# Kernel tuning notes

Hardware: AMD Instinct MI355X
Metric: run time of the kernel (lower is better)

Reference implementation:

```python
import jax, jax.numpy as jnp
import numpy as np

N_E, E_DIM, BETA = 8192, 512, 0.25


def setup_inputs() -> dict:
    key = jax.random.key(0)
    k1, k2 = jax.random.split(key)
    z = jax.random.normal(k1, (16, 1024, E_DIM), dtype=jnp.float32)
    # embedding initialized uniform(-1/n_e, 1/n_e)
    emb_w = jax.random.uniform(k2, (N_E, E_DIM), dtype=jnp.float32,
                               minval=-1.0 / N_E, maxval=1.0 / N_E)
    return {"z": z, "emb_w": emb_w}


def reference(z, emb_w):
    B, T, D = z.shape
    zf = z.reshape(-1, D)  # [BT, D]
    # squared-distance matrix: ||z||^2 + ||e||^2 - 2 z e^T  -> [BT, n_e]
    d = (jnp.sum(zf * zf, axis=1, keepdims=True)
         + jnp.sum(emb_w * emb_w, axis=1)
         - 2.0 * jnp.einsum('bd,nd->bn', zf, emb_w))
    idx = jnp.argmin(d, axis=1)  # [BT]
    z_q = emb_w[idx].reshape(z.shape)  # [B, T, D]
    # legacy=False: beta * commit + codebook term
    loss = (BETA * jnp.mean((jax.lax.stop_gradient(z_q) - z) ** 2)
            + jnp.mean((z_q - jax.lax.stop_gradient(z)) ** 2))
    # straight-through: value equals z_q
    z_q_st = z + jax.lax.stop_gradient(z_q - z)
    idx_out = idx.reshape(B, T)
    v = jnp.var(idx_out.astype(jnp.float32))
    return z_q_st, loss, idx_out, v
```

## Files before the change

kernel.cpp:

```cpp
#include <hip/hip_runtime.h>


#define BT   16384
#define DIMS 512
#define NE   8192
#define NS   4
#define BN   256
#define NTPB (NE / NS / BN)
#define NSTEPS 64

#define LOSS_OFF 8388608
#define IDX_OFF  8388609
#define V_OFF    8404993

#define BEST_OFF  0
#define ENORM_OFF 131072
#define SUMS_OFF  163840
#define CNT_OFF   163864

typedef __attribute__((ext_vector_type(8))) short short8;
typedef __attribute__((ext_vector_type(4))) float floatx4;

#define AS1(p) ((const __attribute__((address_space(1))) void*)(p))
#define AS3(p) ((__attribute__((address_space(3))) void*)(p))

__device__ __forceinline__ unsigned f2bf(float f) {
    unsigned u = __builtin_bit_cast(unsigned, f);
    u += 0x7FFFu + ((u >> 16) & 1u);
    return u >> 16;
}

__global__ __launch_bounds__(256) void prep_kernel(
    const float* __restrict__ z, const float* __restrict__ emb,
    ushort* __restrict__ zh, ushort* __restrict__ ehh,
    float* __restrict__ enorm, unsigned long long* __restrict__ best,
    double* __restrict__ sums, unsigned* __restrict__ counter)
{
    const int lane = threadIdx.x & 63, w = threadIdx.x >> 6;
    const int b = blockIdx.x;
    if (b < NE / 4) {
        const int row = b * 4 + w;
        const float4* p = (const float4*)(emb + (size_t)row * DIMS + lane * 8);
        float4 a = p[0], bb = p[1];
        uint4 h;
        h.x = f2bf(a.x) | (f2bf(a.y) << 16);
        h.y = f2bf(a.z) | (f2bf(a.w) << 16);
        h.z = f2bf(bb.x) | (f2bf(bb.y) << 16);
        h.w = f2bf(bb.z) | (f2bf(bb.w) << 16);
        *(uint4*)(ehh + (size_t)row * DIMS + lane * 8) = h;
        float s = a.x*a.x + a.y*a.y + a.z*a.z + a.w*a.w
                + bb.x*bb.x + bb.y*bb.y + bb.z*bb.z + bb.w*bb.w;
        #pragma unroll
        for (int off = 32; off > 0; off >>= 1) s += __shfl_down(s, off, 64);
        if (lane == 0) enorm[row] = s;
    } else {
        const int row = (b - NE / 4) * 4 + w;
        const float4* p = (const float4*)(z + (size_t)row * DIMS + lane * 8);
        float4 a = p[0], bb = p[1];
        uint4 h;
        h.x = f2bf(a.x) | (f2bf(a.y) << 16);
        h.y = f2bf(a.z) | (f2bf(a.w) << 16);
        h.z = f2bf(bb.x) | (f2bf(bb.y) << 16);
        h.w = f2bf(bb.z) | (f2bf(bb.w) << 16);
        *(uint4*)(zh + (size_t)row * DIMS + lane * 8) = h;
    }
    const int gid = b * 256 + threadIdx.x;
    if (gid < BT) best[gid] = 0xFFFFFFFFFFFFFFFFULL;
    if (gid == 0) { sums[0] = 0.0; sums[1] = 0.0; sums[2] = 0.0; *counter = 0u; }
}


#define LOADB(AB_, NJ0)                                                        \
    _Pragma("unroll")                                                          \
    for (int j2 = 0; j2 < 2; j2++) {                                           \
        b[j2][0] = *(const short8*)&lds[16384u + (AB_) + bro + ((NJ0) + j2) * 1024 + pxo0]; \
        b[j2][1] = *(const short8*)&lds[16384u + (AB_) + bro + ((NJ0) + j2) * 1024 + pxo1]; \
    }

#define PHASE_MID(NJ0)                                                         \
    __builtin_amdgcn_sched_barrier(0);                                         \
    __builtin_amdgcn_s_barrier();                                              \
    asm volatile("s_waitcnt lgkmcnt(0)" ::: "memory");                         \
    __builtin_amdgcn_sched_barrier(0);                                         \
    __builtin_amdgcn_s_setprio(1);                                             \
    _Pragma("unroll")                                                          \
    for (int kk = 0; kk < 2; kk++)                                             \
        _Pragma("unroll")                                                      \
        for (int j2 = 0; j2 < 2; j2++)                                         \
            _Pragma("unroll")                                                  \
            for (int mi = 0; mi < 4; mi++)                                     \
                acc[mi][(NJ0) + j2] = __builtin_amdgcn_mfma_f32_16x16x32_bf16( \
                    a[mi][kk], b[j2][kk], acc[mi][(NJ0) + j2], 0, 0, 0);       \
    __builtin_amdgcn_s_setprio(0);

#define STAGE_A(SA_, H_) do {                                                  \
    const int sa_ = (SA_);                                                     \
    if (sa_ < NSTEPS) {                                                        \
        const int k0_ = (sa_ & 7) * 64;                                        \
        const unsigned al_ = (unsigned)(sa_ & 1) * 32768u                      \
                           + (unsigned)((((H_) * 128) + w * 8) * 64);          \
        const ushort* g_ = zA + (size_t)((H_) * 128) * DIMS + soff + k0_;      \
        __builtin_amdgcn_global_load_lds(AS1(g_), AS3(&lds[al_]), 16, 0, 0);   \
        __builtin_amdgcn_global_load_lds(AS1(g_ + (size_t)64 * DIMS),          \
                                         AS3(&lds[al_ + 64 * 64]), 16, 0, 0);  \
    }                                                                          \
} while (0)

#define STAGE_B(SB_, H_) do {                                                  \
    const int sb_ = (SB_);                                                     \
    if (sb_ < NSTEPS) {                                                        \
        const int k0_ = (sb_ & 7) * 64;                                        \
        const unsigned bl_ = 16384u + (unsigned)(sb_ & 1) * 32768u             \
                           + (unsigned)((((H_) * 128) + w * 8) * 64);          \
        const ushort* g_ = eh + (size_t)(nsN + (sb_ >> 3) * 256 + (H_) * 128) * DIMS \
                         + soff + k0_;                                         \
        __builtin_amdgcn_global_load_lds(AS1(g_), AS3(&lds[bl_]), 16, 0, 0);   \
        __builtin_amdgcn_global_load_lds(AS1(g_ + (size_t)64 * DIMS),          \
                                         AS3(&lds[bl_ + 64 * 64]), 16, 0, 0);  \
    }                                                                          \
} while (0)

#define STEP(S_, AB_, TM_) do {                                                \
    const int s_ = (S_);                                                       \
    short8 a[4][2], b[2][2];                                                   \
         \
    _Pragma("unroll")                                                          \
    for (int mi = 0; mi < 4; mi++) {                                           \
        a[mi][0] = *(const short8*)&lds[(AB_) + aro + mi * 1024 + pxo0];       \
        a[mi][1] = *(const short8*)&lds[(AB_) + aro + mi * 1024 + pxo1];       \
    }                                                                          \
    LOADB(AB_, 0)                                                              \
    STAGE_B(s_ + 1, 0);                                                        \
    PHASE_MID(0)                                                               \
    __builtin_amdgcn_s_barrier();                                              \
                                   \
    LOADB(AB_, 2)                                                              \
    STAGE_B(s_ + 1, 1);                                                        \
    PHASE_MID(2)                                                               \
    __builtin_amdgcn_s_barrier();                                              \
      \
    LOADB(AB_, 4)                                                              \
    STAGE_A(s_ + 2, 0);                                                        \
    PHASE_MID(4)                                                               \
    __builtin_amdgcn_s_barrier();                                              \
            \
    LOADB(AB_, 6)                                                              \
    STAGE_A(s_ + 2, 1);                                                        \
    PHASE_MID(6)                                                               \
    if ((TM_) == 0) asm volatile("s_waitcnt vmcnt(4)" ::: "memory");           \
    else if ((TM_) == 1) asm volatile("s_waitcnt vmcnt(0)" ::: "memory");      \
    __builtin_amdgcn_s_barrier();                                              \
} while (0)

__global__ __launch_bounds__(512, 2) void argmin_mfma(
    const ushort* __restrict__ zh, const ushort* __restrict__ eh,
    const float* __restrict__ enorm, unsigned long long* __restrict__ best)
{
    __shared__ __align__(16) ushort lds[69632];
    float* elds = (float*)&lds[65536];

    const int t = threadIdx.x;
    const int w = t >> 6, lane = t & 63;
    const int quad = lane >> 4, l15 = lane & 15;

    const int d = blockIdx.x;
    const int xcd = d & 7, slot = d >> 3;
    const int ns = xcd >> 1;
    const int mt = slot * 2 + (xcd & 1);
    const int m0 = mt * 256;
    const int nsN = ns * (NTPB * BN);

    const int wrow = (w & 3) * 64;
    const int wcol = (w >> 2) * 128;

    {
        float4 v = *(const float4*)(enorm + nsN + t * 4);
        *(float4*)(elds + t * 4) = v;
    }
    __syncthreads();

    const int l8 = lane >> 3, c8 = lane & 7;
    const int chunk = c8 ^ l8;
    const int soff = (w * 8 + l8) * DIMS + chunk * 8;
    const ushort* zA = zh + (size_t)m0 * DIMS;

    const int pxo0 = (quad ^ (l15 & 7)) * 8;
    const int pxo1 = ((4 + quad) ^ (l15 & 7)) * 8;
    const int aro = (wrow + l15) * 64;
    const int bro = (wcol + l15) * 64;

    floatx4 acc[4][8];
    #pragma unroll
    for (int mi = 0; mi < 4; mi++)
        #pragma unroll
        for (int nj = 0; nj < 8; nj++)
            acc[mi][nj] = (floatx4){0.f, 0.f, 0.f, 0.f};

    float bs[16];
    int   bn_[16];
    #pragma unroll
    for (int k = 0; k < 16; k++) { bs[k] = 3.4e38f; bn_[k] = 0; }

    STAGE_A(0, 0); STAGE_A(0, 1);
    STAGE_B(0, 0); STAGE_B(0, 1);
    STAGE_A(1, 0); STAGE_A(1, 1);
    asm volatile("s_waitcnt vmcnt(4)" ::: "memory");
    __builtin_amdgcn_s_barrier();

    for (int sp = 0; sp < NSTEPS; sp += 2) {
        const int tm1 = (sp != NSTEPS - 2) ? 0 : 1;
        const int tm2 = (sp != NSTEPS - 2) ? 0 : 2;
        STEP(sp, 0u, tm1);
        STEP(sp + 1, 32768u, tm2);

        if ((sp & 7) == 6) {
            const int nt = sp >> 3;
            const int ebase = nt * 256 + wcol + l15;
            const int nbase = nsN + nt * 256 + wcol + l15;
            #pragma unroll
            for (int nj = 0; nj < 8; nj++) {
                const float en = elds[ebase + nj * 16];
                const int n = nbase + nj * 16;
                #pragma unroll
                for (int mi = 0; mi < 4; mi++) {
                    #pragma unroll
                    for (int r = 0; r < 4; r++) {
                        const int k = mi * 4 + r;
                        const float sc = fmaf(-2.0f, acc[mi][nj][r], en);
                        if (sc < bs[k]) { bs[k] = sc; bn_[k] = n; }
                    }
                    acc[mi][nj] = (floatx4){0.f, 0.f, 0.f, 0.f};
                }
            }
        }
    }

    #pragma unroll
    for (int mi = 0; mi < 4; mi++)
        #pragma unroll
        for (int r = 0; r < 4; r++) {
            const int k = mi * 4 + r;
            unsigned su = __builtin_bit_cast(unsigned, bs[k]);
            su = (su & 0x80000000u) ? ~su : (su | 0x80000000u);
            unsigned long long key = ((unsigned long long)su << 32) | (unsigned)bn_[k];
            #pragma unroll
            for (int off = 1; off < 16; off <<= 1) {
                unsigned long long o = __shfl_xor(key, off, 64);
                key = (o < key) ? o : key;
            }
            if (l15 == 0) atomicMin(&best[m0 + wrow + mi * 16 + quad * 4 + r], key);
        }
}

__global__ __launch_bounds__(256) void gather_loss_kernel(
    const float* __restrict__ z, const float* __restrict__ emb,
    const unsigned long long* __restrict__ best,
    float* __restrict__ out, double* __restrict__ sums, unsigned* __restrict__ counter)
{
    __shared__ int sIdx[32];
    __shared__ double red[4];
    const int t = threadIdx.x;
    const int row0 = blockIdx.x * 32;
    double myIdxSum = 0.0, myIdxSq = 0.0;
    if (t < 32) {
        int row = row0 + t;
        int idx = (int)(unsigned)(best[row] & 0xFFFFFFFFULL);
        sIdx[t] = idx;
        out[IDX_OFF + row] = (float)idx;
        myIdxSum = (double)idx;
        myIdxSq = (double)idx * (double)idx;
    }
    __syncthreads();
    double acc = 0.0;
    #pragma unroll 4
    for (int i = 0; i < 16; i++) {
        int e = i * 1024 + t * 4;
        int rl = e >> 9;
        int c = e & 511;
        int idx = sIdx[rl];
        float4 zv = *(const float4*)(z + (size_t)(row0 + rl) * DIMS + c);
        float4 ev = *(const float4*)(emb + (size_t)idx * DIMS + c);
        *(float4*)(out + (size_t)(row0 + rl) * DIMS + c) = ev;
        float dx = zv.x - ev.x, dy = zv.y - ev.y;
        float dz = zv.z - ev.z, dw = zv.w - ev.w;
        acc += (double)(dx * dx + dy * dy) + (double)(dz * dz + dw * dw);
    }
    const int lane = t & 63, wv = t >> 6;
    #pragma unroll
    for (int off = 32; off > 0; off >>= 1) {
        acc      += __shfl_down(acc, off, 64);
        myIdxSum += __shfl_down(myIdxSum, off, 64);
        myIdxSq  += __shfl_down(myIdxSq, off, 64);
    }
    if (lane == 0) red[wv] = acc;
    __syncthreads();
    if (t == 0) {
        double tot = red[0] + red[1] + red[2] + red[3];
        atomicAdd(&sums[0], tot);
        atomicAdd(&sums[1], myIdxSum);
        atomicAdd(&sums[2], myIdxSq);
        __threadfence();
        unsigned old = atomicAdd(counter, 1u);
        if (old == gridDim.x - 1) {
            __threadfence();
            double s0 = atomicAdd(&sums[0], 0.0);
            double s1 = atomicAdd(&sums[1], 0.0);
            double s2 = atomicAdd(&sums[2], 0.0);
            out[LOSS_OFF] = (float)(1.25 * s0 / (double)((size_t)BT * DIMS));
            double m = s1 / (double)BT;
            out[V_OFF] = (float)(s2 / (double)BT - m * m);
        }
    }
}

extern "C" void kernel_launch(void* const* d_in, const int* in_sizes, int n_in,
                              void* d_out, int out_size, void* d_ws, size_t ws_size,
                              hipStream_t stream) {
    const float* z = (const float*)d_in[0];
    const float* emb = (const float*)d_in[1];
    float* out = (float*)d_out;
    char* ws = (char*)d_ws;
    unsigned long long* best = (unsigned long long*)(ws + BEST_OFF);
    float* enorm  = (float*)(ws + ENORM_OFF);
    double* sums  = (double*)(ws + SUMS_OFF);
    unsigned* counter = (unsigned*)(ws + CNT_OFF);

    ushort* zh = (ushort*)out;
    ushort* ehh = zh + (size_t)BT * DIMS;

    hipLaunchKernelGGL(prep_kernel, dim3(NE / 4 + BT / 4), dim3(256), 0, stream,
                       z, emb, zh, ehh, enorm, best, sums, counter);
    hipLaunchKernelGGL(argmin_mfma, dim3(256), dim3(512), 0, stream,
                       zh, ehh, enorm, best);
    hipLaunchKernelGGL(gather_loss_kernel, dim3(BT / 32), dim3(256), 0, stream,
                       z, emb, best, out, sums, counter);
}
```

Baseline: 258.4 us.

## Reorder MFMA phases by K-half with inline-asm LDS reads and unconditional staging

Each step's inner loop is restructured so that every phase loads four B fragments for a single K-half and issues 16 MFMAs, in place of two B fragments across both K-halves. The A fragments are now loaded half at a time. LDS reads are emitted as inline-asm ds_read_b128/b32 so the compiler cannot reschedule them. The bounds checks on global-to-LDS staging are dropped by wrapping the step index with &63, so the last steps issue redundant prefetches, and the final vmcnt(0) wait is removed. The aim is to cut per-phase LDS instruction overhead and branch/scheduling cost, at the price of extra global loads at the tail and fewer interleaving opportunities for the compiler.

```diff
diff --git a/kernel.cpp b/kernel.cpp
--- a/kernel.cpp
+++ b/kernel.cpp
@@ -70,85 +70,86 @@
 }
 
 
-#define LOADB(AB_, NJ0)                                                        \
-    _Pragma("unroll")                                                          \
-    for (int j2 = 0; j2 < 2; j2++) {                                           \
-        b[j2][0] = *(const short8*)&lds[16384u + (AB_) + bro + ((NJ0) + j2) * 1024 + pxo0]; \
-        b[j2][1] = *(const short8*)&lds[16384u + (AB_) + bro + ((NJ0) + j2) * 1024 + pxo1]; \
-    }
-
-#define PHASE_MID(NJ0)                                                         \
+__device__ __forceinline__ void dsr_fence() {
+    asm volatile("s_waitcnt lgkmcnt(0)" ::: "memory");
+    __builtin_amdgcn_sched_barrier(0);
+}
+
+#define DSR8(dst, IDX) do {                                                    \
+    unsigned a_ = (unsigned)(size_t)AS3(&lds[IDX]);                            \
+    asm volatile("ds_read_b128 %0, %1" : "=v"(dst) : "v"(a_));                 \
+} while (0)
+
+#define PH_SYNC()                                                              \
     __builtin_amdgcn_sched_barrier(0);                                         \
     __builtin_amdgcn_s_barrier();                                              \
-    asm volatile("s_waitcnt lgkmcnt(0)" ::: "memory");                         \
-    __builtin_amdgcn_sched_barrier(0);                                         \
+    dsr_fence();
+
+#define MFMA16(KK, NJ0)                                                        \
     __builtin_amdgcn_s_setprio(1);                                             \
     _Pragma("unroll")                                                          \
-    for (int kk = 0; kk < 2; kk++)                                             \
+    for (int j2 = 0; j2 < 4; j2++)                                             \
         _Pragma("unroll")                                                      \
-        for (int j2 = 0; j2 < 2; j2++)                                         \
-            _Pragma("unroll")                                                  \
-            for (int mi = 0; mi < 4; mi++)                                     \
-                acc[mi][(NJ0) + j2] = __builtin_amdgcn_mfma_f32_16x16x32_bf16( \
-                    a[mi][kk], b[j2][kk], acc[mi][(NJ0) + j2], 0, 0, 0);       \
+        for (int mi = 0; mi < 4; mi++)                                         \
+            acc[mi][(NJ0) + j2] = __builtin_amdgcn_mfma_f32_16x16x32_bf16(     \
+                a[mi][KK], b[j2], acc[mi][(NJ0) + j2], 0, 0, 0);               \
     __builtin_amdgcn_s_setprio(0);
 
 #define STAGE_A(SA_, H_) do {                                                  \
     const int sa_ = (SA_);                                                     \
-    if (sa_ < NSTEPS) {                                                        \
-        const int k0_ = (sa_ & 7) * 64;                                        \
-        const unsigned al_ = (unsigned)(sa_ & 1) * 32768u                      \
-                           + (unsigned)((((H_) * 128) + w * 8) * 64);          \
-        const ushort* g_ = zA + (size_t)((H_) * 128) * DIMS + soff + k0_;      \
-        __builtin_amdgcn_global_load_lds(AS1(g_), AS3(&lds[al_]), 16, 0, 0);   \
-        __builtin_amdgcn_global_load_lds(AS1(g_ + (size_t)64 * DIMS),          \
-                                         AS3(&lds[al_ + 64 * 64]), 16, 0, 0);  \
-    }                                                                          \
+    const int sc_ = sa_ & 63;                                                  \
+    const unsigned al_ = (unsigned)(sa_ & 1) * 32768u                          \
+                       + (unsigned)((((H_) * 128) + w * 8) * 64);              \
+    const ushort* g_ = zA + (size_t)((H_) * 128) * DIMS + soff                 \
+                     + ((sc_ & 7) * 64);                                       \
+    __builtin_amdgcn_global_load_lds(AS1(g_), AS3(&lds[al_]), 16, 0, 0);       \
+    __builtin_amdgcn_global_load_lds(AS1(g_ + (size_t)64 * DIMS),              \
+                                     AS3(&lds[al_ + 64 * 64]), 16, 0, 0);      \
 } while (0)
 
 #define STAGE_B(SB_, H_) do {                                                  \
     const int sb_ = (SB_);                                                     \
-    if (sb_ < NSTEPS) {                                                        \
-        const int k0_ = (sb_ & 7) * 64;                                        \
-        const unsigned bl_ = 16384u + (unsigned)(sb_ & 1) * 32768u             \
-                           + (unsigned)((((H_) * 128) + w * 8) * 64);          \
-        const ushort* g_ = eh + (size_t)(nsN + (sb_ >> 3) * 256 + (H_) * 128) * DIMS \
-                         + soff + k0_;                                         \
-        __builtin_amdgcn_global_load_lds(AS1(g_), AS3(&lds[bl_]), 16, 0, 0);   \
-        __builtin_amdgcn_global_load_lds(AS1(g_ + (size_t)64 * DIMS),          \
-                                         AS3(&lds[bl_ + 64 * 64]), 16, 0, 0);  \
-    }                                                                          \
+    const int sc_ = sb_ & 63;                                                  \
+    const unsigned bl_ = 16384u + (unsigned)(sb_ & 1) * 32768u                 \
+                       + (unsigned)((((H_) * 128) + w * 8) * 64);              \
+    const ushort* g_ = eh + (size_t)(nsN + (sc_ >> 3) * 256 + (H_) * 128) * DIMS \
+                     + soff + ((sc_ & 7) * 64);                                \
+    __builtin_amdgcn_global_load_lds(AS1(g_), AS3(&lds[bl_]), 16, 0, 0);       \
+    __builtin_amdgcn_global_load_lds(AS1(g_ + (size_t)64 * DIMS),              \
+                                     AS3(&lds[bl_ + 64 * 64]), 16, 0, 0);      \
 } while (0)
 
 #define STEP(S_, AB_, TM_) do {                                                \
     const int s_ = (S_);                                                       \
-    short8 a[4][2], b[2][2];                                                   \
-         \
-    _Pragma("unroll")                                                          \
-    for (int mi = 0; mi < 4; mi++) {                                           \
-        a[mi][0] = *(const short8*)&lds[(AB_) + aro + mi * 1024 + pxo0];       \
-        a[mi][1] = *(const short8*)&lds[(AB_) + aro + mi * 1024 + pxo1];       \
-    }                                                                          \
-    LOADB(AB_, 0)                                                              \
+    short8 a[4][2], b[4];                                                      \
+                      \
+    _Pragma("unroll") for (int mi = 0; mi < 4; mi++)                           \
+        DSR8(a[mi][0], (AB_) + aro + mi * 1024 + pxo0);                        \
+    _Pragma("unroll") for (int j2 = 0; j2 < 4; j2++)                           \
+        DSR8(b[j2], 16384u + (AB_) + bro + j2 * 1024 + pxo0);                  \
     STAGE_B(s_ + 1, 0);                                                        \
-    PHASE_MID(0)                                                               \
-    __builtin_amdgcn_s_barrier();                                              \
-                                   \
-    LOADB(AB_, 2)                                                              \
+    PH_SYNC(); MFMA16(0, 0);                                                   \
+    __builtin_amdgcn_s_barrier();                                              \
+                      \
+    _Pragma("unroll") for (int mi = 0; mi < 4; mi++)                           \
+        DSR8(a[mi][1], (AB_) + aro + mi * 1024 + pxo1);                        \
+    _Pragma("unroll") for (int j2 = 0; j2 < 4; j2++)                           \
+        DSR8(b[j2], 16384u + (AB_) + bro + (4 + j2) * 1024 + pxo0);            \
     STAGE_B(s_ + 1, 1);                                                        \
-    PHASE_MID(2)                                                               \
-    __builtin_amdgcn_s_barrier();                                              \
-      \
-    LOADB(AB_, 4)                                                              \
+    PH_SYNC(); MFMA16(0, 4);                                                   \
+    __builtin_amdgcn_s_barrier();                                              \
+          \
+    _Pragma("unroll") for (int j2 = 0; j2 < 4; j2++)                           \
+        DSR8(b[j2], 16384u + (AB_) + bro + j2 * 1024 + pxo1);                  \
     STAGE_A(s_ + 2, 0);                                                        \
-    PHASE_MID(4)                                                               \
-    __builtin_amdgcn_s_barrier();                                              \
-            \
-    LOADB(AB_, 6)                                                              \
+    PH_SYNC(); MFMA16(1, 0);                                                   \
+    __builtin_amdgcn_s_barrier();                                              \
+        \
+    _Pragma("unroll") for (int j2 = 0; j2 < 4; j2++)                           \
+        DSR8(b[j2], 16384u + (AB_) + bro + (4 + j2) * 1024 + pxo1);            \
     STAGE_A(s_ + 2, 1);                                                        \
-    PHASE_MID(6)                                                               \
+    PH_SYNC(); MFMA16(1, 4);                                                   \
     if ((TM_) == 0) asm volatile("s_waitcnt vmcnt(4)" ::: "memory");           \
-    else if ((TM_) == 1) asm volatile("s_waitcnt vmcnt(0)" ::: "memory");      \
     __builtin_amdgcn_s_barrier();                                              \
 } while (0)
 
@@ -208,25 +209,29 @@
     __builtin_amdgcn_s_barrier();
 
     for (int sp = 0; sp < NSTEPS; sp += 2) {
-        const int tm1 = (sp != NSTEPS - 2) ? 0 : 1;
-        const int tm2 = (sp != NSTEPS - 2) ? 0 : 2;
-        STEP(sp, 0u, tm1);
-        STEP(sp + 1, 32768u, tm2);
+        STEP(sp, 0u, 0);
+        STEP(sp + 1, 32768u, (sp == NSTEPS - 2) ? 2 : 0);
 
         if ((sp & 7) == 6) {
             const int nt = sp >> 3;
-            const int ebase = nt * 256 + wcol + l15;
-            const int nbase = nsN + nt * 256 + wcol + l15;
+            const int eb = nt * 256 + wcol + l15;
+            const int nbase = nsN + eb;
+            float en[8];
             #pragma unroll
             for (int nj = 0; nj < 8; nj++) {
-                const float en = elds[ebase + nj * 16];
+                unsigned a_ = (unsigned)(size_t)AS3(&elds[eb + nj * 16]);
+                asm volatile("ds_read_b32 %0, %1" : "=v"(en[nj]) : "v"(a_));
+            }
+            dsr_fence();
+            #pragma unroll
+            for (int nj = 0; nj < 8; nj++) {
                 const int n = nbase + nj * 16;
                 #pragma unroll
                 for (int mi = 0; mi < 4; mi++) {
                     #pragma unroll
                     for (int r = 0; r < 4; r++) {
                         const int k = mi * 4 + r;
-                        const float sc = fmaf(-2.0f, acc[mi][nj][r], en);
+                        const float sc = fmaf(-2.0f, acc[mi][nj][r], en[nj]);
                         if (sc < bs[k]) { bs[k] = sc; bn_[k] = n; }
                     }
                     acc[mi][nj] = (floatx4){0.f, 0.f, 0.f, 0.f};
```

Result: no change. 258.0 us (-0.2%).
